# Kernel tuning notes

Measured on AMD Instinct MI355X. Metric: run time of the kernel, lower is better.

The kernel has to match this reference:

```python
import jax, jax.numpy as jnp
import numpy as np

B = 1024   # batch
N = 512    # points per sample (fixed by Linear(512,128))
G = 32     # voxel grid side (fixed: 5 stride-2 convs must reach 1^3)
CH = [1, 4, 16, 32, 64, 128]
BN_EPS = 1e-5


def _basis():
    # PointEmbed sinusoidal basis: hidden_dim=48 -> 8 freqs per axis, [3, 24]
    e = (2.0 ** np.arange(8)).astype(np.float32) * np.pi
    z = np.zeros(8, np.float32)
    b = np.stack([np.concatenate([e, z, z]),
                  np.concatenate([z, e, z]),
                  np.concatenate([z, z, e])])
    return jnp.asarray(b)


def setup_inputs() -> dict:
    key = jax.random.key(0)
    ks = jax.random.split(key, 16)
    inp = {
        "voxels": jax.random.normal(ks[0], (B, 1, G, G, G), jnp.float32),
        "centers": jax.random.uniform(ks[1], (B, N, 3), jnp.float32) * 2.0 - 1.0,
    }
    for i in range(5):
        cin, cout = CH[i], CH[i + 1]
        inp[f"W{i+1}"] = jax.random.normal(ks[2 + i], (cout, cin, 3, 3, 3), jnp.float32) * 0.05
        inp[f"b{i+1}"] = jnp.zeros((cout,), jnp.float32)
        inp[f"g{i+1}"] = jnp.ones((cout,), jnp.float32)
        inp[f"beta{i+1}"] = jnp.zeros((cout,), jnp.float32)
    inp["pe_w"] = jax.random.normal(ks[7], (51, 128), jnp.float32) * 0.05  # Linear(48+3, 128)
    inp["pe_b"] = jnp.zeros((128,), jnp.float32)
    inp["f1_w"] = jax.random.normal(ks[8], (128, 1), jnp.float32) * 0.05   # ff_128_1
    inp["f1_b"] = jnp.zeros((1,), jnp.float32)
    inp["f2_w"] = jax.random.normal(ks[9], (512, 128), jnp.float32) * 0.05  # ff_512_128
    inp["f2_b"] = jnp.zeros((128,), jnp.float32)
    return inp


def _conv_bn_relu(x, W, b, g, beta):
    # SparseConv3d(k=3, s=2, p=1) on fully-occupied grid == dense conv; BN in batch-stats mode
    y = jax.lax.conv_general_dilated(
        x, W, window_strides=(2, 2, 2), padding=[(1, 1)] * 3,
        dimension_numbers=("NCDHW", "OIDHW", "NCDHW"))
    y = y + b[None, :, None, None, None]
    m = jnp.mean(y, axis=(0, 2, 3, 4), keepdims=True)
    v = jnp.var(y, axis=(0, 2, 3, 4), keepdims=True)
    y = (y - m) * jax.lax.rsqrt(v + BN_EPS)
    y = y * g[None, :, None, None, None] + beta[None, :, None, None, None]
    return jax.nn.relu(y)


def reference(voxels, centers,
              W1, b1, g1, beta1, W2, b2, g2, beta2, W3, b3, g3, beta3,
              W4, b4, g4, beta4, W5, b5, g5, beta5,
              pe_w, pe_b, f1_w, f1_b, f2_w, f2_b):
    # --- PointEmbed branch ---
    basis = _basis()                                      # [3, 24]
    proj = jnp.einsum("bnd,de->bne", centers, basis)      # [B, N, 24]
    emb = jnp.concatenate([jnp.sin(proj), jnp.cos(proj), centers], axis=2)  # [B, N, 51]
    xc = emb @ pe_w + pe_b                                # [B, N, 128]
    xc = (xc @ f1_w + f1_b)[..., 0]                       # [B, N=512]
    xc = xc @ f2_w + f2_b                                 # [B, 128]
    # --- sparse conv stack (dense-occupancy equivalent) ---
    x = voxels
    for W, b, g, be in ((W1, b1, g1, beta1), (W2, b2, g2, beta2),
                        (W3, b3, g3, beta3), (W4, b4, g4, beta4),
                        (W5, b5, g5, beta5)):
        x = _conv_bn_relu(x, W, b, g, be)
    x = x.reshape(-1, 128)                                # [B,128,1,1,1] -> [B,128]
    return x + xc
```

## Files before the change

### kernel.cpp

```cpp
#include <hip/hip_runtime.h>
#include <hip/hip_bf16.h>

#ifndef M_PI
#define M_PI 3.14159265358979323846
#endif

#define BN_EPS 1e-5f

#define OFF_Y1   0ull
#define OFF_Y2   16777216ull
#define OFF_Y3   25165824ull
#define OFF_Y4   27262976ull
#define OFF_Y5   27787264ull
#define OFF_S    27918336ull
#define OFF_W2G  28442624ull
#define OFF_W3G  28444352ull
#define OFF_W5G  28458176ull
#define OFF_U    28523712ull
#define OFF_SP1  28523776ull
#define OFF_SP2  28524288ull
#define OFF_SP3  28526336ull
#define OFF_SP4  28530432ull
#define OFF_SP5  28538624ull
#define SP_TOTAL 31232
#define OFF_W4G  OFF_Y1

__device__ __forceinline__ float wred(float v) {
    for (int m = 32; m; m >>= 1) v += __shfl_xor(v, m, 64);
    return v;
}

__device__ __forceinline__ void async_copy16(const float* g, float* l) {
    __builtin_amdgcn_global_load_lds((const __attribute__((address_space(1))) void*)g,
                                     (__attribute__((address_space(3))) void*)l,
                                     16, 0, 0);
}

__global__ void k_prep_w(const float* __restrict__ W2, const float* __restrict__ W3,
                         const float* __restrict__ W5,
                         float* __restrict__ w2g, float* __restrict__ w3g,
                         float* __restrict__ w5g) {
    int idx = blockIdx.x * 256 + threadIdx.x;
    if (idx < 1728) {
        int co = idx & 15; int r = idx >> 4; int tap = r % 27; int ci = r / 27;
        w2g[idx] = W2[(co * 4 + ci) * 27 + tap];
        return;
    }
    idx -= 1728;
    if (idx < 13824) {
        int co = idx & 31; int r = idx >> 5; int tap = r % 27; int ci = r / 27;
        w3g[idx] = W3[(co * 16 + ci) * 27 + tap];
        return;
    }
    idx -= 13824;
    if (idx < 65536) {
        int co = idx & 127; int k = idx >> 7;
        int dx = k & 1, dy = (k >> 1) & 1, dz = (k >> 2) & 1, ci = k >> 3;
        w5g[idx] = W5[(co * 64 + ci) * 27 + (dz + 1) * 9 + (dy + 1) * 3 + (dx + 1)];
    }
}

__global__ void k_prep_w4(const float* __restrict__ W4, float* __restrict__ w4g) {
    int idx = blockIdx.x * 256 + threadIdx.x;
    if (idx < 55296) {
        int co = idx & 63; int r = idx >> 6;
        int tap = r % 27, ci = r / 27;
        w4g[idx] = W4[(co * 32 + ci) * 27 + tap];
    }
}

__global__ void k_prep_u(const float* __restrict__ pe_w, const float* __restrict__ pe_b,
                         const float* __restrict__ f1_w, const float* __restrict__ f1_b,
                         float* __restrict__ u) {
    int t = threadIdx.x;
    if (t < 51) {
        float acc = 0.f;
        for (int j = 0; j < 128; j++) acc += pe_w[t * 128 + j] * f1_w[j];
        u[t] = acc;
    } else if (t == 51) {
        float acc = f1_b[0];
        for (int j = 0; j < 128; j++) acc += pe_b[j] * f1_w[j];
        u[51] = acc;
    }
}

__global__ __launch_bounds__(256) void k_pe(const float* __restrict__ centers,
                                            const float* __restrict__ u,
                                            float* __restrict__ s) {
    __shared__ float us[52];
    int t = threadIdx.x;
    if (t < 52) us[t] = u[t];
    __syncthreads();
    int idx = blockIdx.x * 256 + t;
    float c3[3];
    c3[0] = centers[idx * 3 + 0];
    c3[1] = centers[idx * 3 + 1];
    c3[2] = centers[idx * 3 + 2];
    float acc = us[51] + c3[0] * us[48] + c3[1] * us[49] + c3[2] * us[50];
#pragma unroll
    for (int a = 0; a < 3; a++) {
#pragma unroll
        for (int f = 0; f < 8; f++) {
            float ang = c3[a] * (float)(M_PI * (double)(1 << f));
            float sv, cv;
            sincosf(ang, &sv, &cv);
            acc += sv * us[a * 8 + f] + cv * us[24 + a * 8 + f];
        }
    }
    s[idx] = acc;
}

__global__ __launch_bounds__(256) void k_c1(const float* __restrict__ vox,
                                            const float* __restrict__ W1,
                                            const float* __restrict__ b1,
                                            float* __restrict__ y1,
                                            float* __restrict__ sp1) {
    __shared__ __align__(16) float slab[9 * 1024];
    __shared__ __align__(16) float wl[112];
    __shared__ float red2[32];
    int bid = blockIdx.x;
    int b = bid >> 1, q = bid & 1;
    int t = threadIdx.x;
    const float* vb = vox + (size_t)b * 32768;
    int wu = __builtin_amdgcn_readfirstlane(t >> 6);

    if (t < 108) { int tap = t >> 2, co = t & 3; wl[t] = W1[co * 27 + tap]; }
    if (q == 0) ((float4*)slab)[t] = make_float4(0.f, 0.f, 0.f, 0.f);

    int p0 = 16 * q;
    int s0 = q ? 7 : 0;
    {
        int s = s0;
        for (int i = 0; i < 5; i++) {
            int p = p0 - 1 + i;
            if (p >= 0) async_copy16(vb + p * 1024 + t * 4, slab + s * 1024 + wu * 256);
            s++; if (s == 9) s = 0;
        }
    }
    int yo = t >> 4, xo = t & 15;
    int e = 2 * xo;
    int eA = (e >= 2) ? e - 2 : 0;
    float mx0 = xo ? 1.f : 0.f;
    int iyc[3]; float myv[3];
#pragma unroll
    for (int ky = 0; ky < 3; ky++) {
        int iy = 2 * yo + ky - 1;
        myv[ky] = (iy < 0) ? 0.f : 1.f;
        iyc[ky] = (iy < 0) ? 0 : iy;
    }
    float bb0 = b1[0], bb1 = b1[1], bb2 = b1[2], bb3 = b1[3];
    float sums[4] = {0.f, 0.f, 0.f, 0.f}, sqs[4] = {0.f, 0.f, 0.f, 0.f};

    asm volatile("s_waitcnt vmcnt(0)" ::: "memory");
    __syncthreads();

    int s_win = s0;
    for (int j = 0; j < 4; j++) {
        int zq = 4 * q + j;
        if (j < 3) {
            int sp = s_win + 5; if (sp >= 9) sp -= 9;
            for (int i = 0; i < 4; i++) {
                int p = 4 * zq + 4 + i;
                async_copy16(vb + p * 1024 + t * 4, slab + sp * 1024 + wu * 256);
                sp++; if (sp == 9) sp = 0;
            }
        }
        int P[5];
        {
            int s = s_win;
#pragma unroll
            for (int i = 0; i < 5; i++) { P[i] = s * 1024; s++; if (s == 9) s = 0; }
        }
        float a0[4] = {bb0, bb1, bb2, bb3};
        float a1[4] = {bb0, bb1, bb2, bb3};
#pragma unroll
        for (int kz = 0; kz < 3; kz++) {
            const float* pz0 = slab + P[kz];
            const float* pz1 = slab + P[kz + 2];
#pragma unroll
            for (int ky = 0; ky < 3; ky++) {
                int ro = iyc[ky] * 32;
                float2 xa0 = *(const float2*)(pz0 + ro + eA);
                float2 xb0 = *(const float2*)(pz0 + ro + e);
                float2 xa1 = *(const float2*)(pz1 + ro + eA);
                float2 xb1 = *(const float2*)(pz1 + ro + e);
                float m1 = myv[ky], m0 = m1 * mx0;
                const float* wt = wl + (kz * 9 + ky * 3) * 4;
                float4 w0 = *(const float4*)(wt);
                float4 w1 = *(const float4*)(wt + 4);
                float4 w2 = *(const float4*)(wt + 8);
                float v00 = xa0.y * m0, v01 = xb0.x * m1, v02 = xb0.y * m1;
                float v10 = xa1.y * m0, v11 = xb1.x * m1, v12 = xb1.y * m1;
                a0[0] += v00 * w0.x + v01 * w1.x + v02 * w2.x;
                a0[1] += v00 * w0.y + v01 * w1.y + v02 * w2.y;
                a0[2] += v00 * w0.z + v01 * w1.z + v02 * w2.z;
                a0[3] += v00 * w0.w + v01 * w1.w + v02 * w2.w;
                a1[0] += v10 * w0.x + v11 * w1.x + v12 * w2.x;
                a1[1] += v10 * w0.y + v11 * w1.y + v12 * w2.y;
                a1[2] += v10 * w0.z + v11 * w1.z + v12 * w2.z;
                a1[3] += v10 * w0.w + v11 * w1.w + v12 * w2.w;
            }
        }
        size_t base = (size_t)b * 16384 + (size_t)(2 * zq) * 256 + t;
#pragma unroll
        for (int c = 0; c < 4; c++) {
            y1[base + c * 4096] = a0[c];
            y1[base + c * 4096 + 256] = a1[c];
            sums[c] += a0[c] + a1[c];
            sqs[c] += a0[c] * a0[c] + a1[c] * a1[c];
        }
        s_win += 4; if (s_win >= 9) s_win -= 9;
        asm volatile("s_waitcnt vmcnt(0)" ::: "memory");
        __syncthreads();
    }
    int lane = t & 63, w = t >> 6;
#pragma unroll
    for (int c = 0; c < 4; c++) { sums[c] = wred(sums[c]); sqs[c] = wred(sqs[c]); }
    if (lane == 0) {
#pragma unroll
        for (int c = 0; c < 4; c++) { red2[w * 8 + c] = sums[c]; red2[w * 8 + 4 + c] = sqs[c]; }
    }
    __syncthreads();
    if (t < 8) {
        int c = t >> 1, isq = t & 1;
        float acc = red2[isq * 4 + c] + red2[8 + isq * 4 + c] +
                    red2[16 + isq * 4 + c] + red2[24 + isq * 4 + c];
        atomicAdd(&sp1[(2 * c + isq) * 64 + (bid & 63)], acc);
    }
}

__global__ __launch_bounds__(256) void k_c2(const float* __restrict__ y1,
                                            const float* __restrict__ w2g,
                                            const float* __restrict__ b2,
                                            const float* __restrict__ g1,
                                            const float* __restrict__ be1,
                                            const float* __restrict__ sp1,
                                            float* __restrict__ y2,
                                            float* __restrict__ sp2) {
    __shared__ __align__(16) float slab[9216];
    __shared__ float adl[8];
    __shared__ float red[8];
    int t = threadIdx.x;
    int bid = blockIdx.x;
    int b = bid >> 1, q = bid & 1;
    int w = t >> 6, lane = t & 63;
    int wu = __builtin_amdgcn_readfirstlane(w);
    const float* yb = y1 + (size_t)b * 16384;
    if (q == 0) ((float4*)slab)[t] = make_float4(0.f, 0.f, 0.f, 0.f);
    {
        const float* srcb = yb + wu * 4096 + ((lane ^ ((lane >> 3) & 7)) << 2);
        for (int p = (q ? 0 : 1); p < 9; p++) {
            int zi = 8 * q - 1 + p;
            async_copy16(srcb + zi * 256, slab + p * 1024 + wu * 256);
        }
    }
    for (int row = w; row < 8; row += 4) {
        float v = wred(sp1[row * 64 + lane]);
        if (lane == 0) red[row] = v;
    }
    __syncthreads();
    if (t < 4) {
        float cnt = 4194304.0f;
        float m = red[2 * t] / cnt;
        float var = red[2 * t + 1] / cnt - m * m;
        float a = g1[t] * rsqrtf(var + BN_EPS);
        adl[t] = a; adl[4 + t] = be1[t] - m * a;
    }
    asm volatile("s_waitcnt vmcnt(0)" ::: "memory");
    __syncthreads();
    int yo = lane >> 3, xo = lane & 7;
    float my0 = yo ? 1.f : 0.f, mx0 = xo ? 1.f : 0.f;
    float mzw = (q == 0 && w == 0) ? 0.f : 1.f;
    int yb3[3], xr3[3], xv3[3];
#pragma unroll
    for (int k = 0; k < 3; k++) {
        int yi = 2 * yo + k - 1; int yc = yi < 0 ? 0 : yi;
        yb3[k] = yc * 16; xr3[k] = ((yc >> 1) & 7) << 2;
        int xi = 2 * xo + k - 1; xv3[k] = xi < 0 ? 0 : xi;
    }
    float aa[4], dd[4];
#pragma unroll
    for (int c = 0; c < 4; c++) { aa[c] = adl[c]; dd[c] = adl[4 + c]; }
    float acc[16];
#pragma unroll
    for (int c = 0; c < 16; c++) acc[c] = b2[c];
    for (int ci = 0; ci < 4; ci++) {
        float a = aa[ci], d = dd[ci];
        const float* pb = slab + ci * 256;
        const float* wci = w2g + ci * 432;
#pragma unroll
        for (int kz = 0; kz < 3; kz++) {
            const float* pl = pb + (2 * w + kz) * 1024;
#pragma unroll
            for (int ky = 0; ky < 3; ky++) {
                int A = yb3[ky]; int xr = xr3[ky];
#pragma unroll
                for (int kx = 0; kx < 3; kx++) {
                    float v = pl[(A + xv3[kx]) ^ xr];
                    float vb = fmaxf(a * v + d, 0.f);
                    if (kz == 0) vb *= mzw;
                    if (ky == 0) vb *= my0;
                    if (kx == 0) vb *= mx0;
                    const float* wr = wci + (kz * 9 + ky * 3 + kx) * 16;
#pragma unroll
                    for (int c = 0; c < 16; c++) acc[c] += vb * wr[c];
                }
            }
        }
    }
    int zo = 4 * q + w;
    size_t ob = (size_t)b * 8192 + zo * 64 + lane;
#pragma unroll
    for (int c = 0; c < 16; c++) y2[ob + c * 512] = acc[c];
    int slot = bid & 63;
#pragma unroll
    for (int c = 0; c < 16; c++) {
        float s_ = wred(acc[c]), q_ = wred(acc[c] * acc[c]);
        if (lane == 0) {
            atomicAdd(&sp2[(2 * c) * 64 + slot], s_);
            atomicAdd(&sp2[(2 * c + 1) * 64 + slot], q_);
        }
    }
}

__global__ __launch_bounds__(256) void k_c3(const float* __restrict__ y2,
                                            const float* __restrict__ w3g,
                                            const float* __restrict__ b3,
                                            const float* __restrict__ g2,
                                            const float* __restrict__ be2,
                                            const float* __restrict__ sp2,
                                            float* __restrict__ y3,
                                            float* __restrict__ sp3) {
    __shared__ __align__(16) float in3[8192];
    __shared__ float adl[32], red[32];
    int t = threadIdx.x;
    int b = blockIdx.x;
    int w = t >> 6, lane = t & 63;
    int wu = __builtin_amdgcn_readfirstlane(w);
    const float* yb = y2 + (size_t)b * 8192;
    for (int j = 0; j < 8; j++) {
        int s = ((j << 2) + (lane >> 4)) & 7;
        async_copy16(yb + wu * 2048 + j * 256 + ((lane ^ s) << 2),
                     in3 + wu * 2048 + j * 256);
    }
    for (int row = w; row < 32; row += 4) {
        float v = wred(sp2[row * 64 + lane]);
        if (lane == 0) red[row] = v;
    }
    __syncthreads();
    if (t < 16) {
        float cnt = 524288.0f;
        float m = red[2 * t] / cnt;
        float var = red[2 * t + 1] / cnt - m * m;
        float a = g2[t] * rsqrtf(var + BN_EPS);
        adl[t] = a; adl[16 + t] = be2[t] - m * a;
    }
    asm volatile("s_waitcnt vmcnt(0)" ::: "memory");
    __syncthreads();
    int px = lane & 3, py = (lane >> 2) & 3, pz = lane >> 4;
    float mz0 = pz ? 1.f : 0.f, my0 = py ? 1.f : 0.f, mx0 = px ? 1.f : 0.f;
    int zb3[3], sz3[3], yv3[3], xv3[3];
#pragma unroll
    for (int k = 0; k < 3; k++) {
        int zi = 2 * pz + k - 1; int zc = zi < 0 ? 0 : zi;
        zb3[k] = zc * 64; sz3[k] = zc << 2;
        int yi = 2 * py + k - 1; int yc = yi < 0 ? 0 : yi;
        yv3[k] = yc * 8;
        int xi = 2 * px + k - 1; xv3[k] = xi < 0 ? 0 : xi;
    }
    int coh = wu & 1, cih = wu >> 1;
    int cgo = coh * 16;
    float acc[16];
#pragma unroll
    for (int c = 0; c < 16; c++) acc[c] = 0.f;
    for (int cii = 0; cii < 8; cii++) {
        int ci = cih * 8 + cii;
        float a = adl[ci], d = adl[16 + ci];
        const float* base = in3 + ci * 512;
        const float* wci = w3g + ci * 864 + cgo;
#pragma unroll
        for (int kz = 0; kz < 3; kz++) {
            int A1 = zb3[kz], sz = sz3[kz];
#pragma unroll
            for (int ky = 0; ky < 3; ky++) {
                int A2 = A1 + yv3[ky];
#pragma unroll
                for (int kx = 0; kx < 3; kx++) {
                    float v = base[(A2 + xv3[kx]) ^ sz];
                    float vb = fmaxf(a * v + d, 0.f);
                    if (kz == 0) vb *= mz0;
                    if (ky == 0) vb *= my0;
                    if (kx == 0) vb *= mx0;
                    const float* wr = wci + (kz * 9 + ky * 3 + kx) * 32;
#pragma unroll
                    for (int c = 0; c < 16; c++) acc[c] += vb * wr[c];
                }
            }
        }
    }
    __syncthreads();
    if (wu >= 2) {
        float* pp = in3 + (wu & 1) * 1280 + lane * 20;
#pragma unroll
        for (int c4 = 0; c4 < 4; c4++)
            *(float4*)(pp + c4 * 4) = make_float4(acc[c4*4], acc[c4*4+1], acc[c4*4+2], acc[c4*4+3]);
    }
    __syncthreads();
    if (wu < 2) {
        const float* pp = in3 + wu * 1280 + lane * 20;
#pragma unroll
        for (int c = 0; c < 16; c++) acc[c] += pp[c] + b3[cgo + c];
        size_t ob = (size_t)b * 2048 + lane;
#pragma unroll
        for (int c = 0; c < 16; c++) y3[ob + (size_t)(cgo + c) * 64] = acc[c];
        int slot = b & 63;
#pragma unroll
        for (int c = 0; c < 16; c++) {
            float s_ = wred(acc[c]), q_ = wred(acc[c] * acc[c]);
            if (lane == 0) {
                atomicAdd(&sp3[(2 * (cgo + c)) * 64 + slot], s_);
                atomicAdd(&sp3[(2 * (cgo + c) + 1) * 64 + slot], q_);
            }
        }
    }
}

__global__ __launch_bounds__(256) void k_c4(const float* __restrict__ y3,
                                            const float* __restrict__ w4g,
                                            const float* __restrict__ b4,
                                            const float* __restrict__ g3,
                                            const float* __restrict__ be3,
                                            const float* __restrict__ sp3,
                                            float* __restrict__ y4,
                                            float* __restrict__ sp4) {
    __shared__ __align__(16) float in4[16416];
    __shared__ float adb[64], red[64];
    int t = threadIdx.x;
    int bid = blockIdx.x;
    int bq = bid >> 2, coq = bid & 3;
    int w = t >> 6, lane = t & 63;
    int wu = __builtin_amdgcn_readfirstlane(w);
#pragma unroll
    for (int h = 0; h < 2; h++) {
        int bs2 = wu * 2 + h;
        const float* src = y3 + (size_t)(bq * 8 + bs2) * 2048 + lane * 4;
        for (int j = 0; j < 8; j++)
            async_copy16(src + j * 256, in4 + bs2 * 2052 + j * 256);
    }
    for (int row = w; row < 64; row += 4) {
        float v = wred(sp3[row * 64 + lane]);
        if (lane == 0) red[row] = v;
    }
    __syncthreads();
    if (t < 32) {
        float cnt = 65536.0f;
        float m = red[2 * t] / cnt;
        float var = red[2 * t + 1] / cnt - m * m;
        float a = g3[t] * rsqrtf(var + BN_EPS);
        adb[t] = a; adb[32 + t] = be3[t] - m * a;
    }
    asm volatile("s_waitcnt vmcnt(0)" ::: "memory");
    __syncthreads();
    int bs = lane >> 3, pos = lane & 7;
    int pz = pos >> 2, py = (pos >> 1) & 1, px = pos & 1;
    int z0 = 2 * pz - 1; if (z0 < 0) z0 = 0;
    int y0 = 2 * py - 1; if (y0 < 0) y0 = 0;
    int x0 = 2 * px - 1; if (x0 < 0) x0 = 0;
    int zo_[3] = {z0 * 16, 2 * pz * 16, (2 * pz + 1) * 16};
    int yo_[3] = {y0 * 4, 2 * py * 4, (2 * py + 1) * 4};
    int xo_[3] = {x0, 2 * px, 2 * px + 1};
    float mz = pz ? 1.f : 0.f, my = py ? 1.f : 0.f, mx = px ? 1.f : 0.f;
    float acc[16];
#pragma unroll
    for (int c = 0; c < 16; c++) acc[c] = 0.f;
    const float* inb = in4 + bs * 2052;
    for (int cii = 0; cii < 8; cii++) {
        int ci = wu * 8 + cii;
        float a = adb[ci], d = adb[32 + ci];
        const float* inc = inb + ci * 64;
        const float* wcb = w4g + ci * 1728 + coq * 16;
#pragma unroll
        for (int kz = 0; kz < 3; kz++)
#pragma unroll
            for (int ky = 0; ky < 3; ky++)
#pragma unroll
                for (int kx = 0; kx < 3; kx++) {
                    float v = inc[zo_[kz] + yo_[ky] + xo_[kx]];
                    float vb = fmaxf(a * v + d, 0.f);
                    if (kz == 0) vb *= mz;
                    if (ky == 0) vb *= my;
                    if (kx == 0) vb *= mx;
                    const float* wr = wcb + (kz * 9 + ky * 3 + kx) * 64;
#pragma unroll
                    for (int c = 0; c < 16; c++) acc[c] += vb * wr[c];
                }
    }
    __syncthreads();
    if (wu > 0) {
        float* pp = in4 + (wu - 1) * 1280 + lane * 20;
#pragma unroll
        for (int c4 = 0; c4 < 4; c4++)
            *(float4*)(pp + c4 * 4) = make_float4(acc[c4*4], acc[c4*4+1], acc[c4*4+2], acc[c4*4+3]);
    }
    __syncthreads();
    if (wu == 0) {
#pragma unroll
        for (int p = 0; p < 3; p++) {
            const float* pp = in4 + p * 1280 + lane * 20;
#pragma unroll
            for (int c = 0; c < 16; c++) acc[c] += pp[c];
        }
        int bfull = bq * 8 + bs;
        size_t ob = (size_t)bfull * 512 + pos;
        int slot = bid & 63;
#pragma unroll
        for (int c = 0; c < 16; c++) {
            float vv = acc[c] + b4[coq * 16 + c];
            y4[ob + (size_t)(coq * 16 + c) * 8] = vv;
            acc[c] = vv;
        }
#pragma unroll
        for (int c = 0; c < 16; c++) {
            float s_ = wred(acc[c]), q_ = wred(acc[c] * acc[c]);
            if (lane == 0) {
                atomicAdd(&sp4[(2 * (coq * 16 + c)) * 64 + slot], s_);
                atomicAdd(&sp4[(2 * (coq * 16 + c) + 1) * 64 + slot], q_);
            }
        }
    }
}

__global__ __launch_bounds__(512) void k_c5(const float* __restrict__ y4,
                                            const float* __restrict__ w5g,
                                            const float* __restrict__ b5,
                                            const float* __restrict__ g4,
                                            const float* __restrict__ be4,
                                            const float* __restrict__ sp4,
                                            float* __restrict__ y5,
                                            float* __restrict__ sp5) {
    __shared__ __align__(16) float A[2048];
    __shared__ float P[512];
    __shared__ float ad[128], red[128];
    int t = threadIdx.x;
    int bq = blockIdx.x;
    int w = t >> 6, lane = t & 63;
    for (int row = w; row < 128; row += 8) {
        float v = wred(sp4[row * 64 + lane]);
        if (lane == 0) red[row] = v;
    }
    __syncthreads();
    if (t < 64) {
        float cnt = 8192.0f;
        float m = red[2 * t] / cnt;
        float var = red[2 * t + 1] / cnt - m * m;
        float a = g4[t] * rsqrtf(var + BN_EPS);
        ad[t] = a; ad[64 + t] = be4[t] - m * a;
    }
    __syncthreads();
    {
        int bs = t >> 7, k0 = (t & 127) << 2;
        float4 vv = *(const float4*)(y4 + (size_t)(bq * 4 + bs) * 512 + k0);
        int ci = k0 >> 3;
        float a = ad[ci], d = ad[64 + ci];
        float4 o;
        o.x = fmaxf(a * vv.x + d, 0.f);
        o.y = fmaxf(a * vv.y + d, 0.f);
        o.z = fmaxf(a * vv.z + d, 0.f);
        o.w = fmaxf(a * vv.w + d, 0.f);
        *(float4*)(A + bs * 512 + k0) = o;
    }
    __syncthreads();
    int bs = w & 3, kh = w >> 2;
    float acc0 = 0.f, acc1 = 0.f;
    const float* Ab = A + bs * 512 + kh * 256;
    const float* wp = w5g + kh * 32768 + lane * 2;
#pragma unroll 8
    for (int k = 0; k < 256; k++) {
        float2 wv = *(const float2*)(wp + k * 128);
        float av = Ab[k];
        acc0 += av * wv.x;
        acc1 += av * wv.y;
    }
    if (kh == 0) {
        P[bs * 128 + lane * 2] = acc0;
        P[bs * 128 + lane * 2 + 1] = acc1;
    }
    __syncthreads();
    if (kh == 1) {
        float f0 = acc0 + P[bs * 128 + lane * 2] + b5[lane * 2];
        float f1 = acc1 + P[bs * 128 + lane * 2 + 1] + b5[lane * 2 + 1];
        *(float2*)(y5 + (size_t)(bq * 4 + bs) * 128 + lane * 2) = make_float2(f0, f1);
        P[bs * 128 + lane * 2] = f0;
        P[bs * 128 + lane * 2 + 1] = f1;
    }
    __syncthreads();
    if (t < 128) {
        float s = 0.f, q = 0.f;
        for (int bb = 0; bb < 4; bb++) {
            float vv = P[bb * 128 + t];
            s += vv; q += vv * vv;
        }
        int slot = bq & 63;
        atomicAdd(&sp5[(2 * t) * 64 + slot], s);
        atomicAdd(&sp5[(2 * t + 1) * 64 + slot], q);
    }
}

__global__ __launch_bounds__(512) void k_f2(const float* __restrict__ s,
                                            const float* __restrict__ f2w,
                                            const float* __restrict__ f2b,
                                            const float* __restrict__ g5,
                                            const float* __restrict__ be5,
                                            const float* __restrict__ sp5,
                                            const float* __restrict__ y5,
                                            float* __restrict__ out) {
    __shared__ __align__(16) float A[2048];
    __shared__ float P[512];
    __shared__ float ad[256], red[256];
    int t = threadIdx.x;
    int bq = blockIdx.x;
    int w = t >> 6, lane = t & 63;
    for (int row = w; row < 256; row += 8) {
        float v = wred(sp5[row * 64 + lane]);
        if (lane == 0) red[row] = v;
    }
    __syncthreads();
    if (t < 128) {
        float cnt = 1024.0f;
        float m = red[2 * t] / cnt;
        float var = red[2 * t + 1] / cnt - m * m;
        float a = g5[t] * rsqrtf(var + BN_EPS);
        ad[t] = a; ad[128 + t] = be5[t] - m * a;
    }
    {
        int bs = t >> 7, k0 = (t & 127) << 2;
        float4 vv = *(const float4*)(s + (size_t)(bq * 4 + bs) * 512 + k0);
        *(float4*)(A + bs * 512 + k0) = vv;
    }
    __syncthreads();
    int bs = w & 3, kh = w >> 2;
    float acc0 = 0.f, acc1 = 0.f;
    const float* Ab = A + bs * 512 + kh * 256;
    const float* wp = f2w + kh * 32768 + lane * 2;
#pragma unroll 8
    for (int k = 0; k < 256; k++) {
        float2 wv = *(const float2*)(wp + k * 128);
        float av = Ab[k];
        acc0 += av * wv.x;
        acc1 += av * wv.y;
    }
    if (kh == 0) {
        P[bs * 128 + lane * 2] = acc0;
        P[bs * 128 + lane * 2 + 1] = acc1;
    }
    __syncthreads();
    if (kh == 1) {
        int b = bq * 4 + bs;
        int co = lane * 2;
        float2 vy = *(const float2*)(y5 + (size_t)b * 128 + co);
        float f0 = acc0 + P[bs * 128 + co] + f2b[co] +
                   fmaxf(ad[co] * vy.x + ad[128 + co], 0.f);
        float f1 = acc1 + P[bs * 128 + co + 1] + f2b[co + 1] +
                   fmaxf(ad[co + 1] * vy.y + ad[128 + co + 1], 0.f);
        *(float2*)(out + (size_t)b * 128 + co) = make_float2(f0, f1);
    }
}

extern "C" void kernel_launch(void* const* d_in, const int* in_sizes, int n_in,
                              void* d_out, int out_size, void* d_ws, size_t ws_size,
                              hipStream_t stream) {
    const float* vox     = (const float*)d_in[0];
    const float* centers = (const float*)d_in[1];
    const float* W1   = (const float*)d_in[2];
    const float* b1   = (const float*)d_in[3];
    const float* g1   = (const float*)d_in[4];
    const float* be1  = (const float*)d_in[5];
    const float* W2   = (const float*)d_in[6];
    const float* b2   = (const float*)d_in[7];
    const float* g2   = (const float*)d_in[8];
    const float* be2  = (const float*)d_in[9];
    const float* W3   = (const float*)d_in[10];
    const float* b3   = (const float*)d_in[11];
    const float* g3   = (const float*)d_in[12];
    const float* be3  = (const float*)d_in[13];
    const float* W4   = (const float*)d_in[14];
    const float* b4   = (const float*)d_in[15];
    const float* g4   = (const float*)d_in[16];
    const float* be4  = (const float*)d_in[17];
    const float* W5   = (const float*)d_in[18];
    const float* b5   = (const float*)d_in[19];
    const float* g5   = (const float*)d_in[20];
    const float* be5  = (const float*)d_in[21];
    const float* pe_w = (const float*)d_in[22];
    const float* pe_b = (const float*)d_in[23];
    const float* f1_w = (const float*)d_in[24];
    const float* f1_b = (const float*)d_in[25];
    const float* f2_w = (const float*)d_in[26];
    const float* f2_b = (const float*)d_in[27];

    float* ws  = (float*)d_ws;
    float* y1  = ws + OFF_Y1;
    float* y2  = ws + OFF_Y2;
    float* y3  = ws + OFF_Y3;
    float* y4  = ws + OFF_Y4;
    float* y5  = ws + OFF_Y5;
    float* s   = ws + OFF_S;
    float* w2g = ws + OFF_W2G;
    float* w3g = ws + OFF_W3G;
    float* w4g = ws + OFF_W4G;
    float* w5g = ws + OFF_W5G;
    float* u   = ws + OFF_U;
    float* sp1 = ws + OFF_SP1;
    float* sp2 = ws + OFF_SP2;
    float* sp3 = ws + OFF_SP3;
    float* sp4 = ws + OFF_SP4;
    float* sp5 = ws + OFF_SP5;

    hipMemsetAsync((void*)sp1, 0, SP_TOTAL * sizeof(float), stream);
    k_prep_w<<<317, 256, 0, stream>>>(W2, W3, W5, w2g, w3g, w5g);
    k_prep_u<<<1, 64, 0, stream>>>(pe_w, pe_b, f1_w, f1_b, u);
    k_pe<<<2048, 256, 0, stream>>>(centers, u, s);
    k_c1<<<2048, 256, 0, stream>>>(vox, W1, b1, y1, sp1);
    k_c2<<<2048, 256, 0, stream>>>(y1, w2g, b2, g1, be1, sp1, y2, sp2);
    k_prep_w4<<<216, 256, 0, stream>>>(W4, w4g);
    k_c3<<<1024, 256, 0, stream>>>(y2, w3g, b3, g2, be2, sp2, y3, sp3);
    k_c4<<<512, 256, 0, stream>>>(y3, w4g, b4, g3, be3, sp3, y4, sp4);
    k_c5<<<256, 512, 0, stream>>>(y4, w5g, b5, g4, be4, sp4, y5, sp5);
    k_f2<<<256, 512, 0, stream>>>(s, f2_w, f2_b, g5, be5, sp5, y5, (float*)d_out);
}
```

Measured before the change: 315.7 us.

## Stage conv2 weights in LDS, split channels per wave, launder weight pointers

After: 402.8 us. 1.28x slower.

```diff
diff --git a/kernel.cpp b/kernel.cpp
--- a/kernel.cpp
+++ b/kernel.cpp
@@ -34,6 +34,11 @@
     __builtin_amdgcn_global_load_lds((const __attribute__((address_space(1))) void*)g,
                                      (__attribute__((address_space(3))) void*)l,
                                      16, 0, 0);
+}
+
+__device__ __forceinline__ const float* launder_ptr(const float* p) {
+    asm volatile("" : "+v"(p));
+    return p;
 }
 
 __global__ void k_prep_w(const float* __restrict__ W2, const float* __restrict__ W3,
@@ -238,6 +243,7 @@
                                             float* __restrict__ y2,
                                             float* __restrict__ sp2) {
     __shared__ __align__(16) float slab[9216];
+    __shared__ __align__(16) float wl[1728];
     __shared__ float adl[8];
     __shared__ float red[8];
     int t = threadIdx.x;
@@ -254,6 +260,7 @@
             async_copy16(srcb + zi * 256, slab + p * 1024 + wu * 256);
         }
     }
+    for (int i = t; i < 1728; i += 256) wl[i] = w2g[i];
     for (int row = w; row < 8; row += 4) {
         float v = wred(sp1[row * 64 + lane]);
         if (lane == 0) red[row] = v;
@@ -268,9 +275,11 @@
     }
     asm volatile("s_waitcnt vmcnt(0)" ::: "memory");
     __syncthreads();
+    int zp = w >> 1;
+    int cgo = __builtin_amdgcn_readfirstlane((w & 1) * 8);
     int yo = lane >> 3, xo = lane & 7;
     float my0 = yo ? 1.f : 0.f, mx0 = xo ? 1.f : 0.f;
-    float mzw = (q == 0 && w == 0) ? 0.f : 1.f;
+    float mzw = (q == 0 && zp == 0) ? 0.f : 1.f;
     int yb3[3], xr3[3], xv3[3];
 #pragma unroll
     for (int k = 0; k < 3; k++) {
@@ -281,44 +290,59 @@
     float aa[4], dd[4];
 #pragma unroll
     for (int c = 0; c < 4; c++) { aa[c] = adl[c]; dd[c] = adl[4 + c]; }
-    float acc[16];
-#pragma unroll
-    for (int c = 0; c < 16; c++) acc[c] = b2[c];
+    float acc0[8], acc1[8];
+#pragma unroll
+    for (int c = 0; c < 8; c++) { acc0[c] = b2[cgo + c]; acc1[c] = acc0[c]; }
     for (int ci = 0; ci < 4; ci++) {
         float a = aa[ci], d = dd[ci];
-        const float* pb = slab + ci * 256;
-        const float* wci = w2g + ci * 432;
+        const float* pb = slab + ci * 256 + zp * 4096;
+        const float* wci = wl + ci * 432 + cgo;
 #pragma unroll
         for (int kz = 0; kz < 3; kz++) {
-            const float* pl = pb + (2 * w + kz) * 1024;
+            const float* pl = pb + kz * 1024;
 #pragma unroll
             for (int ky = 0; ky < 3; ky++) {
                 int A = yb3[ky]; int xr = xr3[ky];
 #pragma unroll
                 for (int kx = 0; kx < 3; kx++) {
-                    float v = pl[(A + xv3[kx]) ^ xr];
-                    float vb = fmaxf(a * v + d, 0.f);
-                    if (kz == 0) vb *= mzw;
-                    if (ky == 0) vb *= my0;
-                    if (kx == 0) vb *= mx0;
-                    const float* wr = wci + (kz * 9 + ky * 3 + kx) * 16;
-#pragma unroll
-                    for (int c = 0; c < 16; c++) acc[c] += vb * wr[c];
+                    int ad = (A + xv3[kx]) ^ xr;
+                    float v0 = pl[ad];
+                    float v1 = pl[ad + 2048];
+                    float vb0 = fmaxf(a * v0 + d, 0.f);
+                    float vb1 = fmaxf(a * v1 + d, 0.f);
+                    if (kz == 0) vb0 *= mzw;
+                    if (ky == 0) { vb0 *= my0; vb1 *= my0; }
+                    if (kx == 0) { vb0 *= mx0; vb1 *= mx0; }
+                    const float* wt = wci + (kz * 9 + ky * 3 + kx) * 16;
+                    float4 wA = *(const float4*)(wt);
+                    float4 wB = *(const float4*)(wt + 4);
+                    acc0[0] += vb0 * wA.x; acc0[1] += vb0 * wA.y;
+                    acc0[2] += vb0 * wA.z; acc0[3] += vb0 * wA.w;
+                    acc0[4] += vb0 * wB.x; acc0[5] += vb0 * wB.y;
+                    acc0[6] += vb0 * wB.z; acc0[7] += vb0 * wB.w;
+                    acc1[0] += vb1 * wA.x; acc1[1] += vb1 * wA.y;
+                    acc1[2] += vb1 * wA.z; acc1[3] += vb1 * wA.w;
+                    acc1[4] += vb1 * wB.x; acc1[5] += vb1 * wB.y;
+                    acc1[6] += vb1 * wB.z; acc1[7] += vb1 * wB.w;
                 }
             }
         }
     }
-    int zo = 4 * q + w;
-    size_t ob = (size_t)b * 8192 + zo * 64 + lane;
-#pragma unroll
-    for (int c = 0; c < 16; c++) y2[ob + c * 512] = acc[c];
+    int z0 = 4 * q + 2 * zp;
+    size_t ob = (size_t)b * 8192 + (size_t)cgo * 512 + z0 * 64 + lane;
+#pragma unroll
+    for (int c = 0; c < 8; c++) {
+        y2[ob + c * 512] = acc0[c];
+        y2[ob + c * 512 + 64] = acc1[c];
+    }
     int slot = bid & 63;
 #pragma unroll
-    for (int c = 0; c < 16; c++) {
-        float s_ = wred(acc[c]), q_ = wred(acc[c] * acc[c]);
+    for (int c = 0; c < 8; c++) {
+        float s_ = wred(acc0[c] + acc1[c]);
+        float q_ = wred(acc0[c] * acc0[c] + acc1[c] * acc1[c]);
         if (lane == 0) {
-            atomicAdd(&sp2[(2 * c) * 64 + slot], s_);
-            atomicAdd(&sp2[(2 * c + 1) * 64 + slot], q_);
+            atomicAdd(&sp2[(2 * (cgo + c)) * 64 + slot], s_);
+            atomicAdd(&sp2[(2 * (cgo + c) + 1) * 64 + slot], q_);
         }
     }
 }
@@ -370,6 +394,7 @@
     }
     int coh = wu & 1, cih = wu >> 1;
     int cgo = coh * 16;
+    const float* w3l = launder_ptr(w3g);
     float acc[16];
 #pragma unroll
     for (int c = 0; c < 16; c++) acc[c] = 0.f;
@@ -377,7 +402,7 @@
         int ci = cih * 8 + cii;
         float a = adl[ci], d = adl[16 + ci];
         const float* base = in3 + ci * 512;
-        const float* wci = w3g + ci * 864 + cgo;
+        const float* wci = w3l + ci * 864 + cgo;
 #pragma unroll
         for (int kz = 0; kz < 3; kz++) {
             int A1 = zb3[kz], sz = sz3[kz];
@@ -470,6 +495,7 @@
     int yo_[3] = {y0 * 4, 2 * py * 4, (2 * py + 1) * 4};
     int xo_[3] = {x0, 2 * px, 2 * px + 1};
     float mz = pz ? 1.f : 0.f, my = py ? 1.f : 0.f, mx = px ? 1.f : 0.f;
+    const float* w4l = launder_ptr(w4g);
     float acc[16];
 #pragma unroll
     for (int c = 0; c < 16; c++) acc[c] = 0.f;
@@ -478,7 +504,7 @@
         int ci = wu * 8 + cii;
         float a = adb[ci], d = adb[32 + ci];
         const float* inc = inb + ci * 64;
-        const float* wcb = w4g + ci * 1728 + coq * 16;
+        const float* wcb = w4l + ci * 1728 + coq * 16;
 #pragma unroll
         for (int kz = 0; kz < 3; kz++)
 #pragma unroll
```
